# Kernel optimization log

Hardware: AMD Instinct MI355X
Metric: run time of the kernel (lower is better)

The kernel has to match this reference:

```python
import math
import jax, jax.numpy as jnp
import numpy as np

B, L, D, H = 4, 2048, 512, 8
DK = D // H  # d_keys = d_values = 64
KFAC = 3


def setup_inputs() -> dict:
    key = jax.random.key(0)
    ks = jax.random.split(key, 10)
    u_part = min(KFAC * int(math.ceil(math.log(L))), L)  # 24
    scale = 1.0 / math.sqrt(D)
    return {
        "queries": jax.random.normal(ks[0], (B, L, D), jnp.float32),
        "keys": jax.random.normal(ks[1], (B, L, D), jnp.float32),
        "values": jax.random.normal(ks[2], (B, L, D), jnp.float32),
        "index_sample": jax.random.randint(ks[3], (L, u_part), 0, L, jnp.int32),
        "Wq": jax.random.normal(ks[4], (D, D), jnp.float32) * scale,
        "bq": jnp.zeros((D,), jnp.float32),
        "Wk": jax.random.normal(ks[5], (D, D), jnp.float32) * scale,
        "bk": jnp.zeros((D,), jnp.float32),
        "Wv": jax.random.normal(ks[6], (D, D), jnp.float32) * scale,
        "bv": jnp.zeros((D,), jnp.float32),
        "Wo": jax.random.normal(ks[7], (D, D), jnp.float32) * scale,
        "bo": jnp.zeros((D,), jnp.float32),
    }


def reference(queries, keys, values, index_sample, Wq, bq, Wk, bk, Wv, bv, Wo, bo):
    b, q_len, d_out = queries.shape
    k_len = keys.shape[1]
    # projections -> [B, H, L, DK]
    q = (queries @ Wq + bq).reshape(b, q_len, H, DK).transpose(0, 2, 1, 3)
    k = (keys @ Wk + bk).reshape(b, k_len, H, DK).transpose(0, 2, 1, 3)
    v = (values @ Wv + bv).reshape(b, k_len, H, DK).transpose(0, 2, 1, 3)

    n_top = min(KFAC * int(math.ceil(math.log(q_len))), q_len)  # u

    # --- _prob_qk: sampled QK scores to pick sparse queries ---
    # k_sample: [B, H, q_len, sample_k, DK]
    k_sample = k[:, :, index_sample, :]
    q_k_sample = jnp.einsum("bhld,bhlsd->bhls", q, k_sample)
    m = jnp.max(q_k_sample, axis=-1) - jnp.sum(q_k_sample, axis=-1) / k_len
    _, m_top = jax.lax.top_k(m, n_top)  # [B, H, u]

    q_reduce = jnp.take_along_axis(q, m_top[..., None], axis=2)  # [B, H, u, DK]
    scores_top = jnp.einsum("bhud,bhkd->bhuk", q_reduce, k) / math.sqrt(d_out)

    # --- masked (causal) branch: mask_flag=True ---
    causal = jnp.triu(jnp.ones((q_len, k_len), bool), 1)
    indicator = causal[m_top]  # [B, H, u, k_len]
    scores_top = jnp.where(indicator, -jnp.inf, scores_top)

    attn = jax.nn.softmax(scores_top, axis=-1)  # [B, H, u, k_len]
    context = jnp.cumsum(v, axis=2)  # default context for non-selected queries
    attn_values = jnp.einsum("bhuk,bhkd->bhud", attn, v)

    bidx = jnp.arange(b)[:, None, None]
    hidx = jnp.arange(H)[None, :, None]
    context = context.at[bidx, hidx, m_top].set(attn_values)

    # mix=False: transpose back to [B, L, H, DV] then merge heads
    context = context.transpose(0, 2, 1, 3).reshape(b, q_len, H * DK)
    out = context @ Wo + bo  # dropout_rate=0 / inference: identity
    return out
```

## Files before the change

kernel.cpp:

```cpp
#include <hip/hip_runtime.h>
#include <hip/hip_bf16.h>
#include <math.h>

#define Bq 4
#define Lq 2048
#define Dq 512
#define Hq 8
#define DKq 64
#define Uq 24
#define TSCAN 16
#define NTILE (Lq / TSCAN)
#define JCH 256
#define NCH (Lq / JCH)
#define TKCH 8

typedef unsigned short ushort_t;
typedef unsigned long long u64;
typedef __attribute__((ext_vector_type(8))) short bfrag8;
typedef __attribute__((ext_vector_type(4))) float facc4;

__device__ inline ushort_t bf16_rne(float f) {
  unsigned u = __float_as_uint(f);
  u += 0x7FFF + ((u >> 16) & 1);
  return (ushort_t)(u >> 16);
}
__device__ inline float bf16f(ushort_t h) {
  return __uint_as_float(((unsigned)h) << 16);
}
__device__ inline unsigned fkey(float f) {
  unsigned u = __float_as_uint(f);
  return (u & 0x80000000u) ? ~u : (u | 0x80000000u);
}
__device__ __forceinline__ void gl2lds16(const void* g, void* l) {
  __builtin_amdgcn_global_load_lds(
      (const __attribute__((address_space(1))) unsigned*)g,
      (__attribute__((address_space(3))) unsigned*)l, 16, 0, 0);
}

__global__ __launch_bounds__(256) void cast_all(
    const float* __restrict__ xq, const float* __restrict__ xk,
    const float* __restrict__ xv, ushort_t* __restrict__ qh,
    ushort_t* __restrict__ ql, ushort_t* __restrict__ kh,
    ushort_t* __restrict__ kl, ushort_t* __restrict__ vh) {
  int z = blockIdx.y;
  const float* x = z == 0 ? xq : (z == 1 ? xk : xv);
  ushort_t* hi = z == 0 ? qh : (z == 1 ? kh : vh);
  ushort_t* lo = z == 0 ? ql : kl;
  int t = blockIdx.x * 256 + threadIdx.x;
  float4 v = *(const float4*)&x[(size_t)t * 4];
  ushort_t h0 = bf16_rne(v.x), h1 = bf16_rne(v.y), h2 = bf16_rne(v.z),
           h3 = bf16_rne(v.w);
  ushort4 hh = {h0, h1, h2, h3};
  *(ushort4*)&hi[(size_t)t * 4] = hh;
  if (z < 2) {
    ushort4 ll = {bf16_rne(v.x - bf16f(h0)), bf16_rne(v.y - bf16f(h1)),
                  bf16_rne(v.z - bf16f(h2)), bf16_rne(v.w - bf16f(h3))};
    *(ushort4*)&lo[(size_t)t * 4] = ll;
  }
}

__global__ __launch_bounds__(256) void transpose_cast4(
    const float* __restrict__ W0, const float* __restrict__ W1,
    const float* __restrict__ W2, const float* __restrict__ W3,
    ushort_t* __restrict__ T0h, ushort_t* __restrict__ T0l,
    ushort_t* __restrict__ T1h, ushort_t* __restrict__ T1l,
    ushort_t* __restrict__ T2h, ushort_t* __restrict__ T3h) {
  __shared__ float tile[32][33];
  int z = blockIdx.z;
  const float* W = z == 0 ? W0 : (z == 1 ? W1 : (z == 2 ? W2 : W3));
  ushort_t* Th = z == 0 ? T0h : (z == 1 ? T1h : (z == 2 ? T2h : T3h));
  ushort_t* Tl = z == 0 ? T0l : (z == 1 ? T1l : nullptr);
  int k0 = blockIdx.x * 32, n0 = blockIdx.y * 32;
  int tx = threadIdx.x & 31, ty = threadIdx.x >> 5;
  for (int r = ty; r < 32; r += 8)
    tile[tx][r] = W[(size_t)(k0 + r) * 512 + n0 + tx];
  __syncthreads();
  for (int r = ty; r < 32; r += 8) {
    float v = tile[r][tx];
    ushort_t h = bf16_rne(v);
    Th[(size_t)(n0 + r) * 512 + k0 + tx] = h;
    if (Tl) Tl[(size_t)(n0 + r) * 512 + k0 + tx] = bf16_rne(v - bf16f(h));
  }
}

__global__ __launch_bounds__(256) void gemm_qkv(
    const ushort_t* __restrict__ Aqh, const ushort_t* __restrict__ Aql,
    const ushort_t* __restrict__ Akh, const ushort_t* __restrict__ Akl,
    const ushort_t* __restrict__ Avh,
    const ushort_t* __restrict__ Wqh, const ushort_t* __restrict__ Wql,
    const ushort_t* __restrict__ Wkh, const ushort_t* __restrict__ Wkl,
    const ushort_t* __restrict__ Wvh,
    const float* __restrict__ bq, const float* __restrict__ bk,
    const float* __restrict__ bv,
    float* __restrict__ qo, float* __restrict__ ko, float* __restrict__ vo) {
  __shared__ ushort_t Ash[128][32], Asl[128][32];
  __shared__ ushort_t Bsh[128][32], Bsl[128][32];
  int which = blockIdx.z;
  const ushort_t* Ah = which == 0 ? Aqh : (which == 1 ? Akh : Avh);
  const ushort_t* Al = which == 0 ? Aql : Akl;
  const ushort_t* Bh = which == 0 ? Wqh : (which == 1 ? Wkh : Wvh);
  const ushort_t* Bl = which == 0 ? Wql : Wkl;
  const float* bias = which == 0 ? bq : (which == 1 ? bk : bv);
  float* C = which == 0 ? qo : (which == 1 ? ko : vo);
  const bool split = which < 2;

  int bm = blockIdx.x, bn = blockIdx.y;
  int tid = threadIdx.x;
  int wave = tid >> 6, lane = tid & 63;
  int wm = (wave & 1) * 64, wn = (wave >> 1) * 64;
  int quad = lane >> 4, lm = lane & 15;
  int srow = tid >> 2, skq = (tid & 3) * 8;
  facc4 acc[4][4] = {};

  for (int k0 = 0; k0 < 512; k0 += 32) {
#pragma unroll
    for (int p = 0; p < 2; ++p) {
      int row = srow + p * 64;
      size_t ga = (size_t)(bm * 128 + row) * 512 + k0 + skq;
      size_t gb = (size_t)(bn * 128 + row) * 512 + k0 + skq;
      gl2lds16(&Ah[ga], &Ash[row][skq]);
      gl2lds16(&Bh[gb], &Bsh[row][skq]);
      if (split) {
        gl2lds16(&Al[ga], &Asl[row][skq]);
        gl2lds16(&Bl[gb], &Bsl[row][skq]);
      }
    }
    __syncthreads();
    bfrag8 afh[4], afl[4], bfh[4], bfl[4];
#pragma unroll
    for (int mt = 0; mt < 4; ++mt) {
      afh[mt] = *(bfrag8*)&Ash[wm + mt * 16 + lm][quad * 8];
      if (split) afl[mt] = *(bfrag8*)&Asl[wm + mt * 16 + lm][quad * 8];
    }
#pragma unroll
    for (int nt = 0; nt < 4; ++nt) {
      bfh[nt] = *(bfrag8*)&Bsh[wn + nt * 16 + lm][quad * 8];
      if (split) bfl[nt] = *(bfrag8*)&Bsl[wn + nt * 16 + lm][quad * 8];
    }
#pragma unroll
    for (int mt = 0; mt < 4; ++mt)
#pragma unroll
      for (int nt = 0; nt < 4; ++nt) {
        facc4 a = acc[mt][nt];
        a = __builtin_amdgcn_mfma_f32_16x16x32_bf16(afh[mt], bfh[nt], a, 0, 0, 0);
        if (split) {
          a = __builtin_amdgcn_mfma_f32_16x16x32_bf16(afl[mt], bfh[nt], a, 0, 0, 0);
          a = __builtin_amdgcn_mfma_f32_16x16x32_bf16(afh[mt], bfl[nt], a, 0, 0, 0);
        }
        acc[mt][nt] = a;
      }
    __syncthreads();
  }
#pragma unroll
  for (int mt = 0; mt < 4; ++mt)
#pragma unroll
    for (int nt = 0; nt < 4; ++nt) {
      int col = bn * 128 + wn + nt * 16 + lm;
      float bv2 = bias[col];
#pragma unroll
      for (int r = 0; r < 4; ++r) {
        int row = bm * 128 + wm + mt * 16 + quad * 4 + r;
        C[(size_t)row * 512 + col] = acc[mt][nt][r] + bv2;
      }
    }
}

__global__ __launch_bounds__(256) void gemm_bf16(
    const ushort_t* __restrict__ A, const ushort_t* __restrict__ Bt,
    const float* __restrict__ bias, float* __restrict__ C) {
  __shared__ ushort_t As[128][32];
  __shared__ ushort_t Bs[128][32];
  int bm = blockIdx.x, bn = blockIdx.y;
  int tid = threadIdx.x;
  int wave = tid >> 6, lane = tid & 63;
  int wm = (wave & 1) * 64, wn = (wave >> 1) * 64;
  int quad = lane >> 4, lm = lane & 15;
  int srow = tid >> 2, skq = (tid & 3) * 8;
  facc4 acc[4][4] = {};

  for (int k0 = 0; k0 < 512; k0 += 32) {
#pragma unroll
    for (int p = 0; p < 2; ++p) {
      int row = srow + p * 64;
      gl2lds16(&A[(size_t)(bm * 128 + row) * 512 + k0 + skq], &As[row][skq]);
      gl2lds16(&Bt[(size_t)(bn * 128 + row) * 512 + k0 + skq], &Bs[row][skq]);
    }
    __syncthreads();
    bfrag8 af[4], bf[4];
#pragma unroll
    for (int mt = 0; mt < 4; ++mt)
      af[mt] = *(bfrag8*)&As[wm + mt * 16 + lm][quad * 8];
#pragma unroll
    for (int nt = 0; nt < 4; ++nt)
      bf[nt] = *(bfrag8*)&Bs[wn + nt * 16 + lm][quad * 8];
#pragma unroll
    for (int mt = 0; mt < 4; ++mt)
#pragma unroll
      for (int nt = 0; nt < 4; ++nt)
        acc[mt][nt] = __builtin_amdgcn_mfma_f32_16x16x32_bf16(
            af[mt], bf[nt], acc[mt][nt], 0, 0, 0);
    __syncthreads();
  }
#pragma unroll
  for (int mt = 0; mt < 4; ++mt)
#pragma unroll
    for (int nt = 0; nt < 4; ++nt) {
      int col = bn * 128 + wn + nt * 16 + lm;
      float bv = bias[col];
#pragma unroll
      for (int r = 0; r < 4; ++r) {
        int row = bm * 128 + wm + mt * 16 + quad * 4 + r;
        C[(size_t)row * 512 + col] = acc[mt][nt][r] + bv;
      }
    }
}

__global__ __launch_bounds__(256) void compute_m(
    const float* __restrict__ q, const float* __restrict__ k,
    const int* __restrict__ idxs, float* __restrict__ m) {
  int wave = threadIdx.x >> 6, lane = threadIdx.x & 63;
  int lq = lane >> 4, dq = lane & 15;
  int slot = (blockIdx.x * 4 + wave) * 4 + lq;
  int l = slot & (Lq - 1);
  int bh = slot >> 11;
  int h = bh & (Hq - 1), b = bh >> 3;
  float4 qv = *(const float4*)&q[((size_t)b * Lq + l) * Dq + h * DKq + dq * 4];
  const float* kb = &k[(size_t)b * Lq * Dq + h * DKq + dq * 4];
  const int* ib = &idxs[l * Uq];
  float mx = -INFINITY, sm = 0.f;
#pragma unroll
  for (int s = 0; s < Uq; ++s) {
    int j = ib[s];
    float4 kv = *(const float4*)&kb[(size_t)j * Dq];
    float p = qv.x * kv.x + qv.y * kv.y + qv.z * kv.z + qv.w * kv.w;
    p += __shfl_xor(p, 1, 64);
    p += __shfl_xor(p, 2, 64);
    p += __shfl_xor(p, 4, 64);
    p += __shfl_xor(p, 8, 64);
    mx = fmaxf(mx, p);
    sm += p;
  }
  if (dq == 0) m[slot] = mx - sm * (1.0f / Lq);
}

__device__ inline void bitonic256_desc(u64* s, int tid) {
  for (int k = 2; k <= 256; k <<= 1) {
    for (int j = k >> 1; j > 0; j >>= 1) {
      int p = tid ^ j;
      u64 mine = s[tid], other = s[p];
      u64 mx = mine > other ? mine : other;
      u64 mn = mine > other ? other : mine;
      bool dir = (tid & k) == 0;
      bool lower = tid < p;
      u64 res = dir ? (lower ? mx : mn) : (lower ? mn : mx);
      __syncthreads();
      s[tid] = res;
      __syncthreads();
    }
  }
}

__global__ __launch_bounds__(256) void topk_stage1(
    const float* __restrict__ m, u64* __restrict__ cand) {
  __shared__ u64 s[256];
  int bh = blockIdx.x >> 3;
  int ch = blockIdx.x & 7;
  int tid = threadIdx.x;
  int gidx = ch * 256 + tid;
  float v = m[(size_t)bh * Lq + gidx];
  s[tid] = ((u64)fkey(v) << 32) | (u64)(Lq - 1 - gidx);
  __syncthreads();
  bitonic256_desc(s, tid);
  if (tid < Uq) cand[((size_t)bh * TKCH + ch) * Uq + tid] = s[tid];
}

__global__ __launch_bounds__(256) void topk_stage2(
    const u64* __restrict__ cand, int* __restrict__ mtop,
    int* __restrict__ repl) {
  __shared__ u64 s[256];
  __shared__ int mt[Uq];
  int bh = blockIdx.x;
  int tid = threadIdx.x;
  s[tid] = (tid < TKCH * Uq) ? cand[(size_t)bh * TKCH * Uq + tid] : 0ull;
  __syncthreads();
  bitonic256_desc(s, tid);
  if (tid < Uq) {
    int idx = Lq - 1 - (int)(s[tid] & 0xFFFFFFFFull);
    mtop[bh * Uq + tid] = idx;
    mt[tid] = idx;
  }
  __syncthreads();
  for (int l = tid; l < Lq; l += 256) {
    int u = -1;
#pragma unroll
    for (int t = 0; t < Uq; ++t)
      if (mt[t] == l) u = t;
    repl[(size_t)bh * Lq + l] = u;
  }
}

#define JT 256
#define JS 64

__global__ __launch_bounds__(256) void scores_kernel(
    const float* __restrict__ q, const float* __restrict__ k,
    const int* __restrict__ mtop, float* __restrict__ scg) {
  __shared__ float qs[Uq][DKq + 1];
  __shared__ float ks[JS][DKq + 1];
  __shared__ int i0s[Uq];
  int bh = blockIdx.y;
  int jt = blockIdx.x;
  int h = bh & (Hq - 1);
  int b = bh >> 3;
  int tid = threadIdx.x;
  if (tid < Uq) i0s[tid] = mtop[bh * Uq + tid];
  __syncthreads();
  for (int s = tid; s < Uq * 16; s += 256) {
    int u = s >> 4, qd = (s & 15) * 4;
    float4 t = *(const float4*)&q[((size_t)b * Lq + i0s[u]) * Dq + h * DKq + qd];
    qs[u][qd] = t.x; qs[u][qd + 1] = t.y; qs[u][qd + 2] = t.z; qs[u][qd + 3] = t.w;
  }
  int jp = tid & 31;
  int ug = tid >> 5;
  const float scale = 0.044194173824159216f;
  for (int sub = 0; sub < JT / JS; ++sub) {
    int jbase = jt * JT + sub * JS;
    __syncthreads();
    for (int s = tid; s < JS * 16; s += 256) {
      int j = s >> 4, qd = (s & 15) * 4;
      float4 t = *(const float4*)&k[((size_t)b * Lq + jbase + j) * Dq + h * DKq + qd];
      ks[j][qd] = t.x; ks[j][qd + 1] = t.y; ks[j][qd + 2] = t.z; ks[j][qd + 3] = t.w;
    }
    __syncthreads();
    float acc[3][2] = {};
    int j0 = jp * 2, j1 = j0 + 1;
#pragma unroll 8
    for (int d = 0; d < DKq; ++d) {
      float k0 = ks[j0][d], k1 = ks[j1][d];
#pragma unroll
      for (int uu = 0; uu < 3; ++uu) {
        float qv = qs[ug * 3 + uu][d];
        acc[uu][0] += qv * k0;
        acc[uu][1] += qv * k1;
      }
    }
#pragma unroll
    for (int uu = 0; uu < 3; ++uu) {
      int u = ug * 3 + uu;
      scg[((size_t)(bh * Uq + u)) * Lq + jbase + j0] = acc[uu][0] * scale;
      scg[((size_t)(bh * Uq + u)) * Lq + jbase + j1] = acc[uu][1] * scale;
    }
  }
}

__global__ __launch_bounds__(256) void softmax_pv_partial(
    const float* __restrict__ scg, const float* __restrict__ v,
    const int* __restrict__ mtop, float* __restrict__ pmax,
    float* __restrict__ psum, float* __restrict__ pvp) {
  int blk = blockIdx.y;
  int jc = blockIdx.x;
  int bh = blk / Uq;
  int h = bh & (Hq - 1);
  int b = bh >> 3;
  int n = mtop[blk] + 1;
  int j0 = jc * JCH;
  if (j0 >= n) return;
  int cnt = min(JCH, n - j0);
  int tid = threadIdx.x, wave = tid >> 6, lane = tid & 63;
  __shared__ float es[JCH];
  __shared__ float red[4][DKq];
  __shared__ float rr[4];

  const float* row = &scg[(size_t)blk * Lq + j0];
  float mx = (tid < cnt) ? row[tid] : -INFINITY;
#pragma unroll
  for (int off = 32; off; off >>= 1) mx = fmaxf(mx, __shfl_xor(mx, off, 64));
  if (lane == 0) rr[wave] = mx;
  __syncthreads();
  mx = fmaxf(fmaxf(rr[0], rr[1]), fmaxf(rr[2], rr[3]));
  __syncthreads();

  float e = (tid < cnt) ? __expf(row[tid] - mx) : 0.f;
  es[tid] = e;
  float sm = e;
#pragma unroll
  for (int off = 32; off; off >>= 1) sm += __shfl_xor(sm, off, 64);
  if (lane == 0) rr[wave] = sm;
  __syncthreads();

  float acc = 0.f;
  const float* vb = &v[((size_t)b * Lq + j0) * Dq + h * DKq + lane];
  int jlo = wave * 64;
  int jhi = min(jlo + 64, cnt);
#pragma unroll 4
  for (int j = jlo; j < jhi; ++j) acc += es[j] * vb[(size_t)j * Dq];
  red[wave][lane] = acc;
  __syncthreads();
  if (wave == 0) {
    if (lane == 0) {
      pmax[blk * NCH + jc] = mx;
      psum[blk * NCH + jc] = rr[0] + rr[1] + rr[2] + rr[3];
    }
    pvp[((size_t)blk * NCH + jc) * DKq + lane] =
        red[0][lane] + red[1][lane] + red[2][lane] + red[3][lane];
  }
}

__global__ __launch_bounds__(256) void softmax_pv_combine(
    const float* __restrict__ pmax, const float* __restrict__ psum,
    const float* __restrict__ pvp, const int* __restrict__ mtop,
    float* __restrict__ attnv) {
  int blk = blockIdx.x * 4 + (threadIdx.x >> 6);
  int lane = threadIdx.x & 63;
  int n = mtop[blk] + 1;
  int nc = (n + JCH - 1) / JCH;
  float gmax = -INFINITY;
  for (int c = 0; c < nc; ++c) gmax = fmaxf(gmax, pmax[blk * NCH + c]);
  float tot = 0.f, acc = 0.f;
  for (int c = 0; c < nc; ++c) {
    float w = __expf(pmax[blk * NCH + c] - gmax);
    tot += psum[blk * NCH + c] * w;
    acc += pvp[((size_t)blk * NCH + c) * DKq + lane] * w;
  }
  attnv[(size_t)blk * DKq + lane] = acc / tot;
}

__global__ __launch_bounds__(128) void tile_sum(const float* __restrict__ v,
                                                float* __restrict__ tsum) {
  int blk = blockIdx.x;
  int tile = blk & (NTILE - 1);
  int b = blk >> 7;
  int d4 = threadIdx.x;
  float4 s = {0.f, 0.f, 0.f, 0.f};
  const float* base = &v[((size_t)b * Lq + tile * TSCAN) * Dq + d4 * 4];
#pragma unroll
  for (int r = 0; r < TSCAN; ++r) {
    float4 x = *(const float4*)&base[(size_t)r * Dq];
    s.x += x.x; s.y += x.y; s.z += x.z; s.w += x.w;
  }
  *(float4*)&tsum[((size_t)b * NTILE + tile) * Dq + d4 * 4] = s;
}

__global__ __launch_bounds__(128) void build_context(
    const float* __restrict__ v, const float* __restrict__ tsum,
    const int* __restrict__ repl, const float* __restrict__ attnv,
    ushort_t* __restrict__ ctxh) {
  int blk = blockIdx.x;
  int tile = blk & (NTILE - 1);
  int b = blk >> 7;
  int d4 = threadIdx.x;
  int h = d4 >> 4;
  float4 run = {0.f, 0.f, 0.f, 0.f};
  const float* tb = &tsum[(size_t)b * NTILE * Dq + d4 * 4];
  for (int i = 0; i < tile; ++i) {
    float4 t = *(const float4*)&tb[(size_t)i * Dq];
    run.x += t.x; run.y += t.y; run.z += t.z; run.w += t.w;
  }
  const int* replb = &repl[(size_t)(b * Hq + h) * Lq + tile * TSCAN];
  const float* vb = &v[((size_t)b * Lq + tile * TSCAN) * Dq + d4 * 4];
  ushort_t* cb = &ctxh[((size_t)b * Lq + tile * TSCAN) * Dq + d4 * 4];
  const float* ab = &attnv[(size_t)(b * Hq + h) * Uq * DKq + (d4 & 15) * 4];
#pragma unroll
  for (int r = 0; r < TSCAN; ++r) {
    float4 x = *(const float4*)&vb[(size_t)r * Dq];
    run.x += x.x; run.y += x.y; run.z += x.z; run.w += x.w;
    int u = replb[r];
    float4 val = run;
    if (u >= 0) val = *(const float4*)&ab[(size_t)u * DKq];
    ushort4 o = {bf16_rne(val.x), bf16_rne(val.y), bf16_rne(val.z),
                 bf16_rne(val.w)};
    *(ushort4*)&cb[(size_t)r * Dq] = o;
  }
}

extern "C" void kernel_launch(void* const* d_in, const int* in_sizes, int n_in,
                              void* d_out, int out_size, void* d_ws,
                              size_t ws_size, hipStream_t stream) {
  const float* queries = (const float*)d_in[0];
  const float* keys    = (const float*)d_in[1];
  const float* values  = (const float*)d_in[2];
  const int*   idxs    = (const int*)d_in[3];
  const float* Wq = (const float*)d_in[4];
  const float* bq = (const float*)d_in[5];
  const float* Wk = (const float*)d_in[6];
  const float* bk = (const float*)d_in[7];
  const float* Wv = (const float*)d_in[8];
  const float* bv = (const float*)d_in[9];
  const float* Wo = (const float*)d_in[10];
  const float* bo = (const float*)d_in[11];
  float* out = (float*)d_out;

  const size_t BLD = (size_t)Bq * Lq * Dq;
  char* w = (char*)d_ws;
  float* q    = (float*)w; w += BLD * 4;
  float* k    = (float*)w; w += BLD * 4;
  float* v    = (float*)w; w += BLD * 4;
  float* scg  = (float*)w; w += (size_t)Bq * Hq * Uq * Lq * 4;
  float* m    = (float*)w; w += (size_t)Bq * Hq * Lq * 4;
  float* attnv= (float*)w; w += (size_t)Bq * Hq * Uq * DKq * 4;
  float* tsum = (float*)w; w += (size_t)Bq * NTILE * Dq * 4;
  int* mtop   = (int*)w;   w += Bq * Hq * Uq * 4;
  int* repl   = (int*)w;   w += (size_t)Bq * Hq * Lq * 4;
  float* pmax = (float*)w; w += (size_t)Bq * Hq * Uq * NCH * 4;
  float* psum = (float*)w; w += (size_t)Bq * Hq * Uq * NCH * 4;
  float* pvp  = (float*)w; w += (size_t)Bq * Hq * Uq * NCH * DKq * 4;
  u64* cand   = (u64*)w;   w += (size_t)Bq * Hq * TKCH * Uq * 8;
  ushort_t* ctxh = (ushort_t*)w; w += BLD * 2;
  ushort_t* Aqh = (ushort_t*)w; w += BLD * 2;
  ushort_t* Aql = (ushort_t*)w; w += BLD * 2;
  ushort_t* Akh = (ushort_t*)w; w += BLD * 2;
  ushort_t* Akl = (ushort_t*)w; w += BLD * 2;
  ushort_t* Avh = (ushort_t*)w; w += BLD * 2;
  const size_t WSZ = 512 * 512;
  ushort_t* Wqh = (ushort_t*)w; w += WSZ * 2;
  ushort_t* Wql = (ushort_t*)w; w += WSZ * 2;
  ushort_t* Wkh = (ushort_t*)w; w += WSZ * 2;
  ushort_t* Wkl = (ushort_t*)w; w += WSZ * 2;
  ushort_t* Wvh = (ushort_t*)w; w += WSZ * 2;
  ushort_t* Woh = (ushort_t*)w; w += WSZ * 2;

  {
    dim3 tgrid(16, 16, 4);
    transpose_cast4<<<tgrid, 256, 0, stream>>>(Wq, Wk, Wv, Wo, Wqh, Wql, Wkh,
                                               Wkl, Wvh, Woh);
  }

  {
    dim3 cgrid(BLD / 4 / 256, 3);
    cast_all<<<cgrid, 256, 0, stream>>>(queries, keys, values, Aqh, Aql, Akh,
                                        Akl, Avh);
  }

  {
    dim3 ggrid(64, 4, 3);
    gemm_qkv<<<ggrid, 256, 0, stream>>>(Aqh, Aql, Akh, Akl, Avh, Wqh, Wql,
                                        Wkh, Wkl, Wvh, bq, bk, bv, q, k, v);
  }

  compute_m<<<(Bq * Hq * Lq) / 16, 256, 0, stream>>>(q, k, idxs, m);
  topk_stage1<<<Bq * Hq * TKCH, 256, 0, stream>>>(m, cand);
  topk_stage2<<<Bq * Hq, 256, 0, stream>>>(cand, mtop, repl);

  {
    dim3 sgrid(Lq / JT, Bq * Hq);
    scores_kernel<<<sgrid, 256, 0, stream>>>(q, k, mtop, scg);
  }
  {
    dim3 pgrid(NCH, Bq * Hq * Uq);
    softmax_pv_partial<<<pgrid, 256, 0, stream>>>(scg, v, mtop, pmax, psum, pvp);
    softmax_pv_combine<<<Bq * Hq * Uq / 4, 256, 0, stream>>>(pmax, psum, pvp,
                                                             mtop, attnv);
  }

  tile_sum<<<Bq * NTILE, 128, 0, stream>>>(v, tsum);
  build_context<<<Bq * NTILE, 128, 0, stream>>>(v, tsum, repl, attnv, ctxh);

  {
    dim3 ggrid(64, 4);
    gemm_bf16<<<ggrid, 256, 0, stream>>>(ctxh, Woh, bo, out);
  }
}
```

Baseline: 297.3 us.

## Fuse QK scores into softmax-PV partial and fold combine into context build

The separate scores kernel is removed. Each softmax/PV chunk block now computes its own Q·K dot products from the selected query row and the key chunk, using shuffle reductions, so the full score matrix is no longer written to or read from global memory. Only causal chunks up to the selected query are computed, where the old scores kernel filled all key positions. The combine kernel is also removed, and its cross-chunk max/sum merge is done inline in build_context for each replaced row. This saves two launches and the score and attention-value buffers, but the dot products now run in a shuffle-heavy loop and the merge work is redone per thread inside build_context.

```diff
diff --git a/kernel.cpp b/kernel.cpp
--- a/kernel.cpp
+++ b/kernel.cpp
@@ -299,80 +299,44 @@
   }
 }
 
-#define JT 256
-#define JS 64
-
-__global__ __launch_bounds__(256) void scores_kernel(
+__global__ __launch_bounds__(256) void attn_partial(
     const float* __restrict__ q, const float* __restrict__ k,
-    const int* __restrict__ mtop, float* __restrict__ scg) {
-  __shared__ float qs[Uq][DKq + 1];
-  __shared__ float ks[JS][DKq + 1];
-  __shared__ int i0s[Uq];
-  int bh = blockIdx.y;
-  int jt = blockIdx.x;
-  int h = bh & (Hq - 1);
-  int b = bh >> 3;
-  int tid = threadIdx.x;
-  if (tid < Uq) i0s[tid] = mtop[bh * Uq + tid];
-  __syncthreads();
-  for (int s = tid; s < Uq * 16; s += 256) {
-    int u = s >> 4, qd = (s & 15) * 4;
-    float4 t = *(const float4*)&q[((size_t)b * Lq + i0s[u]) * Dq + h * DKq + qd];
-    qs[u][qd] = t.x; qs[u][qd + 1] = t.y; qs[u][qd + 2] = t.z; qs[u][qd + 3] = t.w;
-  }
-  int jp = tid & 31;
-  int ug = tid >> 5;
-  const float scale = 0.044194173824159216f;
-  for (int sub = 0; sub < JT / JS; ++sub) {
-    int jbase = jt * JT + sub * JS;
-    __syncthreads();
-    for (int s = tid; s < JS * 16; s += 256) {
-      int j = s >> 4, qd = (s & 15) * 4;
-      float4 t = *(const float4*)&k[((size_t)b * Lq + jbase + j) * Dq + h * DKq + qd];
-      ks[j][qd] = t.x; ks[j][qd + 1] = t.y; ks[j][qd + 2] = t.z; ks[j][qd + 3] = t.w;
-    }
-    __syncthreads();
-    float acc[3][2] = {};
-    int j0 = jp * 2, j1 = j0 + 1;
-#pragma unroll 8
-    for (int d = 0; d < DKq; ++d) {
-      float k0 = ks[j0][d], k1 = ks[j1][d];
-#pragma unroll
-      for (int uu = 0; uu < 3; ++uu) {
-        float qv = qs[ug * 3 + uu][d];
-        acc[uu][0] += qv * k0;
-        acc[uu][1] += qv * k1;
-      }
-    }
-#pragma unroll
-    for (int uu = 0; uu < 3; ++uu) {
-      int u = ug * 3 + uu;
-      scg[((size_t)(bh * Uq + u)) * Lq + jbase + j0] = acc[uu][0] * scale;
-      scg[((size_t)(bh * Uq + u)) * Lq + jbase + j1] = acc[uu][1] * scale;
-    }
-  }
-}
-
-__global__ __launch_bounds__(256) void softmax_pv_partial(
-    const float* __restrict__ scg, const float* __restrict__ v,
-    const int* __restrict__ mtop, float* __restrict__ pmax,
-    float* __restrict__ psum, float* __restrict__ pvp) {
+    const float* __restrict__ v, const int* __restrict__ mtop,
+    float* __restrict__ pmax, float* __restrict__ psum,
+    float* __restrict__ pvp) {
   int blk = blockIdx.y;
   int jc = blockIdx.x;
   int bh = blk / Uq;
   int h = bh & (Hq - 1);
   int b = bh >> 3;
-  int n = mtop[blk] + 1;
+  int i0 = mtop[blk];
+  int n = i0 + 1;
   int j0 = jc * JCH;
   if (j0 >= n) return;
   int cnt = min(JCH, n - j0);
   int tid = threadIdx.x, wave = tid >> 6, lane = tid & 63;
+  int jq = lane >> 4, dq = lane & 15;
   __shared__ float es[JCH];
   __shared__ float red[4][DKq];
   __shared__ float rr[4];
-
-  const float* row = &scg[(size_t)blk * Lq + j0];
-  float mx = (tid < cnt) ? row[tid] : -INFINITY;
+  const float scale = 0.044194173824159216f;
+
+  float4 qv = *(const float4*)&q[((size_t)b * Lq + i0) * Dq + h * DKq + dq * 4];
+  const float* kb = &k[(size_t)b * Lq * Dq + h * DKq + dq * 4];
+#pragma unroll 4
+  for (int t = 0; t < 16; ++t) {
+    int jloc = wave * 64 + t * 4 + jq;
+    float4 kv = *(const float4*)&kb[(size_t)(j0 + jloc) * Dq];
+    float p = qv.x * kv.x + qv.y * kv.y + qv.z * kv.z + qv.w * kv.w;
+    p += __shfl_xor(p, 1, 64);
+    p += __shfl_xor(p, 2, 64);
+    p += __shfl_xor(p, 4, 64);
+    p += __shfl_xor(p, 8, 64);
+    if (dq == 0) es[jloc] = p * scale;
+  }
+  __syncthreads();
+
+  float mx = (tid < cnt) ? es[tid] : -INFINITY;
 #pragma unroll
   for (int off = 32; off; off >>= 1) mx = fmaxf(mx, __shfl_xor(mx, off, 64));
   if (lane == 0) rr[wave] = mx;
@@ -380,7 +344,8 @@
   mx = fmaxf(fmaxf(rr[0], rr[1]), fmaxf(rr[2], rr[3]));
   __syncthreads();
 
-  float e = (tid < cnt) ? __expf(row[tid] - mx) : 0.f;
+  float e = (tid < cnt) ? __expf(es[tid] - mx) : 0.f;
+  __syncthreads();
   es[tid] = e;
   float sm = e;
 #pragma unroll
@@ -404,25 +369,6 @@
     pvp[((size_t)blk * NCH + jc) * DKq + lane] =
         red[0][lane] + red[1][lane] + red[2][lane] + red[3][lane];
   }
-}
-
-__global__ __launch_bounds__(256) void softmax_pv_combine(
-    const float* __restrict__ pmax, const float* __restrict__ psum,
-    const float* __restrict__ pvp, const int* __restrict__ mtop,
-    float* __restrict__ attnv) {
-  int blk = blockIdx.x * 4 + (threadIdx.x >> 6);
-  int lane = threadIdx.x & 63;
-  int n = mtop[blk] + 1;
-  int nc = (n + JCH - 1) / JCH;
-  float gmax = -INFINITY;
-  for (int c = 0; c < nc; ++c) gmax = fmaxf(gmax, pmax[blk * NCH + c]);
-  float tot = 0.f, acc = 0.f;
-  for (int c = 0; c < nc; ++c) {
-    float w = __expf(pmax[blk * NCH + c] - gmax);
-    tot += psum[blk * NCH + c] * w;
-    acc += pvp[((size_t)blk * NCH + c) * DKq + lane] * w;
-  }
-  attnv[(size_t)blk * DKq + lane] = acc / tot;
 }
 
 __global__ __launch_bounds__(128) void tile_sum(const float* __restrict__ v,
@@ -443,7 +389,8 @@
 
 __global__ __launch_bounds__(128) void build_context(
     const float* __restrict__ v, const float* __restrict__ tsum,
-    const int* __restrict__ repl, const float* __restrict__ attnv,
+    const int* __restrict__ repl, const float* __restrict__ pmax,
+    const float* __restrict__ psum, const float* __restrict__ pvp,
     ushort_t* __restrict__ ctxh) {
   int blk = blockIdx.x;
   int tile = blk & (NTILE - 1);
@@ -459,14 +406,32 @@
   const int* replb = &repl[(size_t)(b * Hq + h) * Lq + tile * TSCAN];
   const float* vb = &v[((size_t)b * Lq + tile * TSCAN) * Dq + d4 * 4];
   ushort_t* cb = &ctxh[((size_t)b * Lq + tile * TSCAN) * Dq + d4 * 4];
-  const float* ab = &attnv[(size_t)(b * Hq + h) * Uq * DKq + (d4 & 15) * 4];
 #pragma unroll
   for (int r = 0; r < TSCAN; ++r) {
     float4 x = *(const float4*)&vb[(size_t)r * Dq];
     run.x += x.x; run.y += x.y; run.z += x.z; run.w += x.w;
     int u = replb[r];
     float4 val = run;
-    if (u >= 0) val = *(const float4*)&ab[(size_t)u * DKq];
+    if (u >= 0) {
+      int l = tile * TSCAN + r;
+      int blku = (b * Hq + h) * Uq + u;
+      int nc = (l + JCH) / JCH;
+      float gmax = -INFINITY;
+      for (int c = 0; c < nc; ++c) gmax = fmaxf(gmax, pmax[blku * NCH + c]);
+      float tot = 0.f;
+      float4 acc = {0.f, 0.f, 0.f, 0.f};
+      for (int c = 0; c < nc; ++c) {
+        float wgt = __expf(pmax[blku * NCH + c] - gmax);
+        tot += psum[blku * NCH + c] * wgt;
+        float4 pv = *(const float4*)&pvp[((size_t)blku * NCH + c) * DKq +
+                                         (d4 & 15) * 4];
+        acc.x += pv.x * wgt; acc.y += pv.y * wgt;
+        acc.z += pv.z * wgt; acc.w += pv.w * wgt;
+      }
+      float inv = 1.0f / tot;
+      val.x = acc.x * inv; val.y = acc.y * inv;
+      val.z = acc.z * inv; val.w = acc.w * inv;
+    }
     ushort4 o = {bf16_rne(val.x), bf16_rne(val.y), bf16_rne(val.z),
                  bf16_rne(val.w)};
     *(ushort4*)&cb[(size_t)r * Dq] = o;
@@ -495,9 +460,7 @@
   float* q    = (float*)w; w += BLD * 4;
   float* k    = (float*)w; w += BLD * 4;
   float* v    = (float*)w; w += BLD * 4;
-  float* scg  = (float*)w; w += (size_t)Bq * Hq * Uq * Lq * 4;
   float* m    = (float*)w; w += (size_t)Bq * Hq * Lq * 4;
-  float* attnv= (float*)w; w += (size_t)Bq * Hq * Uq * DKq * 4;
   float* tsum = (float*)w; w += (size_t)Bq * NTILE * Dq * 4;
   int* mtop   = (int*)w;   w += Bq * Hq * Uq * 4;
   int* repl   = (int*)w;   w += (size_t)Bq * Hq * Lq * 4;
@@ -542,18 +505,13 @@
   topk_stage2<<<Bq * Hq, 256, 0, stream>>>(cand, mtop, repl);
 
   {
-    dim3 sgrid(Lq / JT, Bq * Hq);
-    scores_kernel<<<sgrid, 256, 0, stream>>>(q, k, mtop, scg);
-  }
-  {
     dim3 pgrid(NCH, Bq * Hq * Uq);
-    softmax_pv_partial<<<pgrid, 256, 0, stream>>>(scg, v, mtop, pmax, psum, pvp);
-    softmax_pv_combine<<<Bq * Hq * Uq / 4, 256, 0, stream>>>(pmax, psum, pvp,
-                                                             mtop, attnv);
+    attn_partial<<<pgrid, 256, 0, stream>>>(q, k, v, mtop, pmax, psum, pvp);
   }
 
   tile_sum<<<Bq * NTILE, 128, 0, stream>>>(v, tsum);
-  build_context<<<Bq * NTILE, 128, 0, stream>>>(v, tsum, repl, attnv, ctxh);
+  build_context<<<Bq * NTILE, 128, 0, stream>>>(v, tsum, repl, pmax, psum,
+                                                pvp, ctxh);
 
   {
     dim3 ggrid(64, 4);
```

Result: slower. 307.3 us (+3.4%).
